# Kernel optimization log

Measured on AMD Instinct MI355X. Metric: run time of the kernel, lower is better.

Reference implementation:

```python
import jax, jax.numpy as jnp
import numpy as np

C, H, W = 64, 32, 32  # feature planes are (1, 64, 32, 32)
M = 1_048_576         # number of query points


def bilinear_sample(plane, coords):
    """torch.nn.functional.grid_sample, mode='bilinear', padding_mode='zeros',
    align_corners=True, for a single plane.
    plane: (C, H, W); coords: (M, 2) with (x, y) in [-1, 1] convention.
    Returns (M, C)."""
    c, h, w = plane.shape
    # align_corners=True mapping: -1 -> 0, +1 -> size-1
    x = (coords[:, 0] + 1.0) * 0.5 * (w - 1)
    y = (coords[:, 1] + 1.0) * 0.5 * (h - 1)
    x0 = jnp.floor(x)
    y0 = jnp.floor(y)
    wx1 = x - x0
    wy1 = y - y0
    wx0 = 1.0 - wx1
    wy0 = 1.0 - wy1

    def gather(xi, yi):
        xi = xi.astype(jnp.int32)
        yi = yi.astype(jnp.int32)
        valid = (xi >= 0) & (xi < w) & (yi >= 0) & (yi < h)  # zeros padding
        xc = jnp.clip(xi, 0, w - 1)
        yc = jnp.clip(yi, 0, h - 1)
        v = plane[:, yc, xc]  # (C, M)
        return jnp.where(valid[None, :], v, 0.0)

    out = (gather(x0, y0) * (wx0 * wy0)[None, :]
           + gather(x0 + 1, y0) * (wx1 * wy0)[None, :]
           + gather(x0, y0 + 1) * (wx0 * wy1)[None, :]
           + gather(x0 + 1, y0 + 1) * (wx1 * wy1)[None, :])
    return out.T  # (M, C)


def setup_inputs() -> dict:
    key = jax.random.key(0)
    ks = jax.random.split(key, 10)
    coordinates = jax.random.normal(ks[0], (1, M, 3), dtype=jnp.float32)
    # tri-plane embeddings: randn * 0.1, shape (1, C, H, W)
    plane_xy = jax.random.normal(ks[1], (1, C, H, W), dtype=jnp.float32) * 0.1
    plane_yz = jax.random.normal(ks[2], (1, C, H, W), dtype=jnp.float32) * 0.1
    plane_xz = jax.random.normal(ks[3], (1, C, H, W), dtype=jnp.float32) * 0.1
    # MLP 64 -> 128 -> 128 -> 1 (torch Linear weight shape = (out, in))
    # layer 0: first_layer_sine_init -> U(-1/64, 1/64)
    w1 = jax.random.uniform(ks[4], (128, 64), jnp.float32, -1.0 / 64, 1.0 / 64)
    b1 = jnp.zeros((128,), jnp.float32)
    # layers 1,2: frequency_init(30) -> U(-sqrt(6/in)/30, sqrt(6/in)/30)
    s2 = np.sqrt(6.0 / 128) / 30.0
    w2 = jax.random.uniform(ks[5], (128, 128), jnp.float32, -s2, s2)
    b2 = jnp.zeros((128,), jnp.float32)
    w3 = jax.random.uniform(ks[6], (1, 128), jnp.float32, -s2, s2)
    b3 = jnp.zeros((1,), jnp.float32)
    return {"coordinates": coordinates, "plane_xy": plane_xy, "plane_yz": plane_yz,
            "plane_xz": plane_xz, "w1": w1, "b1": b1, "w2": w2, "b2": b2,
            "w3": w3, "b3": b3}


def reference(coordinates, plane_xy, plane_yz, plane_xz, w1, b1, w2, b2, w3, b3):
    # coordinates: (1, M, 3); planes have leading batch dim of 1 (torch requires
    # grid batch == plane batch, so batch_size is structurally 1).
    samp = jax.vmap(bilinear_sample, in_axes=(None, 0))
    xy = samp(plane_xy[0], coordinates[..., 0:2])   # (1, M, C)
    yz = samp(plane_yz[0], coordinates[..., 1:3])   # (1, M, C)
    xz = samp(plane_xz[0], coordinates[..., ::2])   # (1, M, C)
    features = xy * yz * xz                          # aggregate_fn='prod'
    h = jax.nn.relu(jnp.einsum('bmc,oc->bmo', features, w1) + b1)
    h = jax.nn.relu(jnp.einsum('bmc,oc->bmo', h, w2) + b2)
    out = jnp.einsum('bmc,oc->bmo', h, w3) + b3      # (1, M, 1)
    return out
```

## Files before the change

### kernel.cpp

```cpp
#include <hip/hip_runtime.h>

#define MPTS 1048576

typedef _Float16 f16;
typedef _Float16 f16x4 __attribute__((ext_vector_type(4)));
typedef _Float16 f16x8 __attribute__((ext_vector_type(8)));
typedef float f32x4 __attribute__((ext_vector_type(4)));

static const size_t OFF_Z    = 0;
static const size_t OFF_CNT  = 64;
static const size_t OFF_PL   = 256;
static const size_t OFF_PLH  = OFF_PL + 786432;
static const size_t OFF_W1H  = OFF_PLH + 393216;
static const size_t OFF_W2H  = OFF_W1H + 16384;
static const size_t OFF_BCNT = OFF_W2H + 32768;
static const size_t OFF_BOFF = OFF_BCNT + 4096;
static const size_t OFF_LIST = OFF_BOFF + 4096;
static const size_t OFF_PC   = OFF_LIST + (size_t)MPTS*4;
static const size_t WS_LIST  = OFF_PC;
static const size_t WS_PC    = OFF_PC + (size_t)MPTS*16;

__device__ __forceinline__ int iclamp(int v, int lo, int hi) {
    return v < lo ? lo : (v > hi ? hi : v);
}
__device__ __forceinline__ int imin(int a, int b) { return a < b ? a : b; }

__device__ __forceinline__ bool isact(float x, float y, float z) {
    float px = fmaf(x, 15.5f, 15.5f);
    float py = fmaf(y, 15.5f, 15.5f);
    float pz = fmaf(z, 15.5f, 15.5f);
    return (px > -1.0f) & (px < 32.0f) & (py > -1.0f) & (py < 32.0f) &
           (pz > -1.0f) & (pz < 32.0f);
}

struct Bi { int o00, o01, o10, o11; float w00, w01, w10, w11; };

__device__ __forceinline__ Bi mkbi(float pa, float pb) {
    float fa = floorf(pa), fb = floorf(pb);
    int ia0 = (int)fa, ib0 = (int)fb;
    int ia1 = ia0 + 1, ib1 = ib0 + 1;
    float wa1 = pa - fa, wa0 = 1.0f - wa1;
    float wb1 = pb - fb, wb0 = 1.0f - wb1;
    float va0 = (ia0 >= 0 && ia0 < 32) ? wa0 : 0.0f;
    float va1 = (ia1 >= 0 && ia1 < 32) ? wa1 : 0.0f;
    float vb0 = (ib0 >= 0 && ib0 < 32) ? wb0 : 0.0f;
    float vb1 = (ib1 >= 0 && ib1 < 32) ? wb1 : 0.0f;
    int ca0 = iclamp(ia0, 0, 31), ca1 = iclamp(ia1, 0, 31);
    int cb0 = iclamp(ib0, 0, 31), cb1 = iclamp(ib1, 0, 31);
    Bi r;
    r.o00 = (cb0 * 32 + ca0) * 64; r.o01 = (cb0 * 32 + ca1) * 64;
    r.o10 = (cb1 * 32 + ca0) * 64; r.o11 = (cb1 * 32 + ca1) * 64;
    r.w00 = va0 * vb0; r.w01 = va1 * vb0; r.w10 = va0 * vb1; r.w11 = va1 * vb1;
    return r;
}

__device__ __forceinline__ float4 lerp4h(const f16* __restrict__ base,
                                         const int4 O, const float4 W) {
    f16x4 g00 = *(const f16x4*)(base + O.x);
    f16x4 g01 = *(const f16x4*)(base + O.y);
    f16x4 g10 = *(const f16x4*)(base + O.z);
    f16x4 g11 = *(const f16x4*)(base + O.w);
    float4 r;
    r.x = fmaf(W.x, (float)g00[0], fmaf(W.y, (float)g01[0], fmaf(W.z, (float)g10[0], W.w * (float)g11[0])));
    r.y = fmaf(W.x, (float)g00[1], fmaf(W.y, (float)g01[1], fmaf(W.z, (float)g10[1], W.w * (float)g11[1])));
    r.z = fmaf(W.x, (float)g00[2], fmaf(W.y, (float)g01[2], fmaf(W.z, (float)g10[2], W.w * (float)g11[2])));
    r.w = fmaf(W.x, (float)g00[3], fmaf(W.y, (float)g01[3], fmaf(W.z, (float)g10[3], W.w * (float)g11[3])));
    return r;
}

__device__ __forceinline__ void samp16(const float* __restrict__ pl,
                                       float pa, float pb, int c0,
                                       float* __restrict__ f, const bool mult) {
    Bi B = mkbi(pa, pb);
    const float4* p00 = (const float4*)(pl + B.o00 + c0);
    const float4* p01 = (const float4*)(pl + B.o01 + c0);
    const float4* p10 = (const float4*)(pl + B.o10 + c0);
    const float4* p11 = (const float4*)(pl + B.o11 + c0);
#pragma unroll
    for (int q = 0; q < 4; ++q) {
        float4 g00 = p00[q], g01 = p01[q], g10 = p10[q], g11 = p11[q];
        float vx = fmaf(B.w00, g00.x, fmaf(B.w01, g01.x, fmaf(B.w10, g10.x, B.w11 * g11.x)));
        float vy = fmaf(B.w00, g00.y, fmaf(B.w01, g01.y, fmaf(B.w10, g10.y, B.w11 * g11.y)));
        float vz = fmaf(B.w00, g00.z, fmaf(B.w01, g01.z, fmaf(B.w10, g10.z, B.w11 * g11.z)));
        float vw = fmaf(B.w00, g00.w, fmaf(B.w01, g01.w, fmaf(B.w10, g10.w, B.w11 * g11.w)));
        if (mult) {
            f[4*q+0] *= vx; f[4*q+1] *= vy; f[4*q+2] *= vz; f[4*q+3] *= vw;
        } else {
            f[4*q+0] = vx; f[4*q+1] = vy; f[4*q+2] = vz; f[4*q+3] = vw;
        }
    }
}

__global__ void k_prep(const float* __restrict__ pxy, const float* __restrict__ pyz,
                       const float* __restrict__ pxz,
                       const float* __restrict__ w1, const float* __restrict__ w2,
                       const float* __restrict__ b1, const float* __restrict__ b2,
                       const float* __restrict__ w3, const float* __restrict__ b3,
                       float* __restrict__ planes, f16* __restrict__ planes_h,
                       f16* __restrict__ w1h, f16* __restrict__ w2h,
                       float* __restrict__ zout) {
    if (blockIdx.x == 864) {
        int p = threadIdx.x;
        if (p >= 128) return;
        float h2p = b2[p];
        for (int o = 0; o < 128; ++o) h2p += w2[p * 128 + o] * fmaxf(b1[o], 0.0f);
        __shared__ float red[128];
        red[p] = fmaxf(h2p, 0.0f) * w3[p];
        __syncthreads();
        for (int s = 64; s > 0; s >>= 1) {
            if (p < s) red[p] += red[p + s];
            __syncthreads();
        }
        if (p == 0) *zout = red[0] + b3[0];
        return;
    }
    int tid = blockIdx.x * 256 + threadIdx.x;
    if (tid < 3 * 65536) {
        int t = tid >> 16;
        int r = tid & 65535;
        int hw = r >> 6;
        int c = r & 63;
        const float* src = (t == 0) ? pxy : ((t == 1) ? pyz : pxz);
        float v = src[c * 1024 + hw];
        planes[tid] = v;
        planes_h[tid] = (f16)v;
    } else if (tid < 3 * 65536 + 8192) {
        int r = tid - 3 * 65536;
        w1h[r] = (f16)w1[r];
    } else {
        int r = tid - (3 * 65536 + 8192);
        w2h[r] = (f16)w2[r];
    }
}

__global__ void k_count(const float* __restrict__ coords, const float* __restrict__ zptr,
                        int* __restrict__ bcnt, float* __restrict__ out) {
    int t = threadIdx.x, bid = blockIdx.x;
    const float4* c4 = (const float4*)coords + 768 * (size_t)bid + 3 * t;
    float4 a = c4[0], b = c4[1], c = c4[2];
    int base = bid * 1024 + t * 4;
    float z = *zptr;
    bool a0 = isact(a.x, a.y, a.z);
    bool a1 = isact(a.w, b.x, b.y);
    bool a2 = isact(b.z, b.w, c.x);
    bool a3 = isact(c.y, c.z, c.w);
    if (!a0) out[base + 0] = z;
    if (!a1) out[base + 1] = z;
    if (!a2) out[base + 2] = z;
    if (!a3) out[base + 3] = z;
    int s = (int)a0 + (int)a1 + (int)a2 + (int)a3;
#pragma unroll
    for (int off = 1; off <= 32; off <<= 1) s += __shfl_xor(s, off, 64);
    __shared__ int wt[4];
    if ((t & 63) == 0) wt[t >> 6] = s;
    __syncthreads();
    if (t == 0) bcnt[bid] = wt[0] + wt[1] + wt[2] + wt[3];
}

__global__ void k_scan(const int* __restrict__ bcnt, int* __restrict__ boff,
                       int* __restrict__ cnt) {
    int t = threadIdx.x, lane = t & 63, wv = t >> 6;
    int mine = bcnt[t];
    int incl = mine;
#pragma unroll
    for (int off = 1; off <= 32; off <<= 1) {
        int v = __shfl_up(incl, off, 64);
        if (lane >= off) incl += v;
    }
    __shared__ int wtot[16];
    if (lane == 63) wtot[wv] = incl;
    __syncthreads();
    int wexcl = 0;
#pragma unroll
    for (int k = 0; k < 16; ++k) wexcl += (k < wv) ? wtot[k] : 0;
    boff[t] = wexcl + incl - mine;
    if (t == 1023) *cnt = wexcl + incl;
}

template<bool PC>
__global__ void k_scatter(const float* __restrict__ coords, const int* __restrict__ boff,
                          int* __restrict__ list, float4* __restrict__ pc4) {
    int t = threadIdx.x, bid = blockIdx.x, lane = t & 63, wv = t >> 6;
    const float4* c4 = (const float4*)coords + 768 * (size_t)bid + 3 * t;
    float4 a = c4[0], b = c4[1], c = c4[2];
    int base = bid * 1024 + t * 4;
    float xs[4] = {a.x, a.w, b.z, c.y};
    float ys[4] = {a.y, b.x, b.w, c.z};
    float zs[4] = {a.z, b.y, c.x, c.w};
    bool act[4];
#pragma unroll
    for (int j = 0; j < 4; ++j) act[j] = isact(xs[j], ys[j], zs[j]);
    int mine = (int)act[0] + (int)act[1] + (int)act[2] + (int)act[3];
    int incl = mine;
#pragma unroll
    for (int off = 1; off <= 32; off <<= 1) {
        int v = __shfl_up(incl, off, 64);
        if (lane >= off) incl += v;
    }
    __shared__ int wtot[4];
    if (lane == 63) wtot[wv] = incl;
    __syncthreads();
    int wexcl = 0;
#pragma unroll
    for (int k = 0; k < 4; ++k) wexcl += (k < wv) ? wtot[k] : 0;
    int pos = boff[bid] + wexcl + incl - mine;
#pragma unroll
    for (int j = 0; j < 4; ++j) {
        if (act[j]) {
            list[pos] = base + j;
            if (PC) {
                float4 p;
                p.x = fmaf(xs[j], 15.5f, 15.5f);
                p.y = fmaf(ys[j], 15.5f, 15.5f);
                p.z = fmaf(zs[j], 15.5f, 15.5f);
                p.w = 0.0f;
                pc4[pos] = p;
            }
            ++pos;
        }
    }
}

__global__ __launch_bounds__(256, 2)
void k_fused(const float4* __restrict__ pc4, const f16* __restrict__ plh,
             const f16* __restrict__ w1h, const f16* __restrict__ w2h,
             const float* __restrict__ b1, const float* __restrict__ b2,
             const float* __restrict__ w3, const float* __restrict__ b3,
             const int* __restrict__ cnt, const int* __restrict__ list,
             float* __restrict__ out) {
    const int n = *cnt;
    const int tile = blockIdx.x;
    if (tile * 64 >= n) return;

    __shared__ __attribute__((aligned(16))) f16 Fs[64 * 64];
    __shared__ __attribute__((aligned(16))) f16 H1s[64 * 128];
    __shared__ float outp[4][64];
    __shared__ int4   BsO[64 * 3];
    __shared__ float4 BsW[64 * 3];

    const int t   = threadIdx.x;
    const int wv  = t >> 6;
    const int l   = t & 63;
    const int l15 = l & 15;
    const int lg  = l >> 4;
    const int ptw = t >> 4;
    const int cq  = t & 15;

    const float b3v = b3[0];

    if ((t & 3) < 3) {
        int pt0 = t >> 2;
        int pl  = t & 3;
        int ic = imin(tile * 64 + pt0, n - 1);
        float4 c = pc4[ic];
        float pa = (pl == 1) ? c.y : c.x;
        float pb = (pl == 0) ? c.y : c.z;
        Bi B = mkbi(pa, pb);
        BsO[pt0 * 3 + pl] = make_int4(B.o00, B.o01, B.o10, B.o11);
        BsW[pt0 * 3 + pl] = make_float4(B.w00, B.w01, B.w10, B.w11);
    }
    __syncthreads();

    const f16* bch = plh + cq * 4;
#pragma unroll
    for (int pass = 0; pass < 4; ++pass) {
        int pt = pass * 16 + ptw;
        float4 s0 = lerp4h(bch,          BsO[pt * 3 + 0], BsW[pt * 3 + 0]);
        float4 s1 = lerp4h(bch + 65536,  BsO[pt * 3 + 1], BsW[pt * 3 + 1]);
        float4 s2 = lerp4h(bch + 131072, BsO[pt * 3 + 2], BsW[pt * 3 + 2]);
        float4 f;
        f.x = (s0.x * s1.x) * s2.x;
        f.y = (s0.y * s1.y) * s2.y;
        f.z = (s0.z * s1.z) * s2.z;
        f.w = (s0.w * s1.w) * s2.w;
        f16x4 pk;
        pk[0] = (f16)f.x; pk[1] = (f16)f.y; pk[2] = (f16)f.z; pk[3] = (f16)f.w;
        *(f16x4*)((char*)Fs + pt * 128 + ((cq * 8) ^ ((pt & 7) << 4))) = pk;
    }
    __syncthreads();

    f16x8 af[4][2];
#pragma unroll
    for (int Mt = 0; Mt < 4; ++Mt) {
        int row = Mt * 16 + l15;
        const char* rb = (const char*)Fs + row * 128;
        int sw = (row & 7) << 4;
        af[Mt][0] = *(const f16x8*)(rb + ((lg * 16) ^ sw));
        af[Mt][1] = *(const f16x8*)(rb + ((64 + lg * 16) ^ sw));
    }

    f16x8 wf1[2][2];
    f16x8 wf2[2][4];
    f32x4 b1q[2], b2q[2], w3q[2];
#pragma unroll
    for (int ntl = 0; ntl < 2; ++ntl) {
        int nrow = (wv * 2 + ntl) * 16 + l15;
        wf1[ntl][0] = *(const f16x8*)(w1h + nrow * 64 + lg * 8);
        wf1[ntl][1] = *(const f16x8*)(w1h + nrow * 64 + 32 + lg * 8);
#pragma unroll
        for (int ks = 0; ks < 4; ++ks)
            wf2[ntl][ks] = *(const f16x8*)(w2h + nrow * 128 + ks * 32 + lg * 8);
        int nb = (wv * 2 + ntl) * 16 + lg * 4;
        b1q[ntl] = *(const f32x4*)(b1 + nb);
        b2q[ntl] = *(const f32x4*)(b2 + nb);
        w3q[ntl] = *(const f32x4*)(w3 + nb);
    }

    f32x4 acc[2][4];
#pragma unroll
    for (int ntl = 0; ntl < 2; ++ntl)
#pragma unroll
        for (int Mt = 0; Mt < 4; ++Mt) acc[ntl][Mt] = b1q[ntl];
    __builtin_amdgcn_s_setprio(1);
#pragma unroll
    for (int Mt = 0; Mt < 4; ++Mt) {
#pragma unroll
        for (int ntl = 0; ntl < 2; ++ntl) {
            acc[ntl][Mt] = __builtin_amdgcn_mfma_f32_16x16x32_f16(wf1[ntl][0], af[Mt][0], acc[ntl][Mt], 0, 0, 0);
            acc[ntl][Mt] = __builtin_amdgcn_mfma_f32_16x16x32_f16(wf1[ntl][1], af[Mt][1], acc[ntl][Mt], 0, 0, 0);
        }
    }
    __builtin_amdgcn_s_setprio(0);

#pragma unroll
    for (int ntl = 0; ntl < 2; ++ntl) {
#pragma unroll
        for (int Mt = 0; Mt < 4; ++Mt) {
            int pt = Mt * 16 + l15;
            int off = (((wv * 2 + ntl) * 32 + lg * 8) ^ ((pt & 7) << 4));
            f16x4 h;
            h[0] = (f16)fmaxf(acc[ntl][Mt][0], 0.0f);
            h[1] = (f16)fmaxf(acc[ntl][Mt][1], 0.0f);
            h[2] = (f16)fmaxf(acc[ntl][Mt][2], 0.0f);
            h[3] = (f16)fmaxf(acc[ntl][Mt][3], 0.0f);
            *(f16x4*)((char*)H1s + pt * 256 + off) = h;
        }
    }
    __syncthreads();

    f32x4 acc2[2][4];
#pragma unroll
    for (int ntl = 0; ntl < 2; ++ntl)
#pragma unroll
        for (int Mt = 0; Mt < 4; ++Mt) acc2[ntl][Mt] = b2q[ntl];
#pragma unroll
    for (int Mt = 0; Mt < 4; ++Mt) {
        int row = Mt * 16 + l15;
        const char* rb = (const char*)H1s + row * 256;
        int sw = (row & 7) << 4;
        f16x8 a0 = *(const f16x8*)(rb + ((lg * 16) ^ sw));
        f16x8 a1 = *(const f16x8*)(rb + ((64 + lg * 16) ^ sw));
        f16x8 a2 = *(const f16x8*)(rb + ((128 + lg * 16) ^ sw));
        f16x8 a3 = *(const f16x8*)(rb + ((192 + lg * 16) ^ sw));
        __builtin_amdgcn_s_setprio(1);
#pragma unroll
        for (int ntl = 0; ntl < 2; ++ntl) {
            acc2[ntl][Mt] = __builtin_amdgcn_mfma_f32_16x16x32_f16(wf2[ntl][0], a0, acc2[ntl][Mt], 0, 0, 0);
            acc2[ntl][Mt] = __builtin_amdgcn_mfma_f32_16x16x32_f16(wf2[ntl][1], a1, acc2[ntl][Mt], 0, 0, 0);
            acc2[ntl][Mt] = __builtin_amdgcn_mfma_f32_16x16x32_f16(wf2[ntl][2], a2, acc2[ntl][Mt], 0, 0, 0);
            acc2[ntl][Mt] = __builtin_amdgcn_mfma_f32_16x16x32_f16(wf2[ntl][3], a3, acc2[ntl][Mt], 0, 0, 0);
        }
        __builtin_amdgcn_s_setprio(0);
    }

#pragma unroll
    for (int Mt = 0; Mt < 4; ++Mt) {
        float s = 0.0f;
#pragma unroll
        for (int ntl = 0; ntl < 2; ++ntl)
#pragma unroll
            for (int r = 0; r < 4; ++r)
                s = fmaf(fmaxf(acc2[ntl][Mt][r], 0.0f), w3q[ntl][r], s);
        s += __shfl_xor(s, 16, 64);
        s += __shfl_xor(s, 32, 64);
        if (lg == 0) outp[wv][Mt * 16 + l15] = s;
    }
    __syncthreads();
    if (t < 64) {
        int gi = tile * 64 + t;
        if (gi < n) {
            float s = outp[0][t] + outp[1][t] + outp[2][t] + outp[3][t] + b3v;
            out[list[gi]] = s;
        }
    }
}

__global__ __launch_bounds__(256, 2)
void k_mlp(const float* __restrict__ coords, const float* __restrict__ planes,
           const f16* __restrict__ w1h, const f16* __restrict__ w2h,
           const float* __restrict__ b1, const float* __restrict__ b2,
           const float* __restrict__ w3, const float* __restrict__ b3,
           const int* __restrict__ cnt, const int* __restrict__ list,
           float* __restrict__ out) {
    const int n = *cnt;
    const int tile = blockIdx.x;
    if (tile * 64 >= n) return;

    __shared__ __attribute__((aligned(16))) f16 Fs[64 * 64];
    __shared__ __attribute__((aligned(16))) f16 H1s[64 * 128];
    __shared__ float outp[4][64];

    const int t   = threadIdx.x;
    const int wv  = t >> 6;
    const int l   = t & 63;
    const int l15 = l & 15;
    const int lg  = l >> 4;

    const float* pl0 = planes;
    const float* pl1 = planes + 65536;
    const float* pl2 = planes + 131072;

    f16x8 wf1[2][2];
    f16x8 wf2[2][4];
    float b1v[2], b2v[2], w3v[2];
#pragma unroll
    for (int ntl = 0; ntl < 2; ++ntl) {
        int nrow = (wv * 2 + ntl) * 16 + l15;
#pragma unroll
        for (int ks = 0; ks < 2; ++ks)
            wf1[ntl][ks] = *(const f16x8*)(w1h + nrow * 64 + ks * 32 + lg * 8);
#pragma unroll
        for (int ks = 0; ks < 4; ++ks)
            wf2[ntl][ks] = *(const f16x8*)(w2h + nrow * 128 + ks * 32 + lg * 8);
        b1v[ntl] = b1[nrow];
        b2v[ntl] = b2[nrow];
        w3v[ntl] = w3[nrow];
    }
    const float b3v = b3[0];

    {
        int pt = t >> 2, c0 = (t & 3) * 16;
        int ic = imin(tile * 64 + pt, n - 1);
        int i = list[ic];
        float px = fmaf(coords[3 * i + 0], 15.5f, 15.5f);
        float py = fmaf(coords[3 * i + 1], 15.5f, 15.5f);
        float pz = fmaf(coords[3 * i + 2], 15.5f, 15.5f);
        float feat[16];
        samp16(pl0, px, py, c0, feat, false);
        samp16(pl1, py, pz, c0, feat, true);
        samp16(pl2, px, pz, c0, feat, true);
        int sw = (pt & 7) << 4;
        char* Fb = (char*)Fs + pt * 128;
        f16x8 pk;
#pragma unroll
        for (int j = 0; j < 8; ++j) pk[j] = (f16)feat[j];
        *(f16x8*)(Fb + ((c0 * 2) ^ sw)) = pk;
#pragma unroll
        for (int j = 0; j < 8; ++j) pk[j] = (f16)feat[8 + j];
        *(f16x8*)(Fb + ((c0 * 2 + 16) ^ sw)) = pk;
    }
    __syncthreads();

    f32x4 acc[2][4];
#pragma unroll
    for (int ntl = 0; ntl < 2; ++ntl) {
        f32x4 ini = {b1v[ntl], b1v[ntl], b1v[ntl], b1v[ntl]};
#pragma unroll
        for (int Mt = 0; Mt < 4; ++Mt) acc[ntl][Mt] = ini;
    }
#pragma unroll
    for (int Mt = 0; Mt < 4; ++Mt) {
        int row = Mt * 16 + l15;
        const char* rb = (const char*)Fs + row * 128;
        int sw = (row & 7) << 4;
        f16x8 a0 = *(const f16x8*)(rb + ((lg * 16) ^ sw));
        f16x8 a1 = *(const f16x8*)(rb + ((64 + lg * 16) ^ sw));
#pragma unroll
        for (int ntl = 0; ntl < 2; ++ntl) {
            acc[ntl][Mt] = __builtin_amdgcn_mfma_f32_16x16x32_f16(a0, wf1[ntl][0], acc[ntl][Mt], 0, 0, 0);
            acc[ntl][Mt] = __builtin_amdgcn_mfma_f32_16x16x32_f16(a1, wf1[ntl][1], acc[ntl][Mt], 0, 0, 0);
        }
    }
#pragma unroll
    for (int ntl = 0; ntl < 2; ++ntl) {
        int ncol = (wv * 2 + ntl) * 16 + l15;
#pragma unroll
        for (int Mt = 0; Mt < 4; ++Mt) {
#pragma unroll
            for (int r = 0; r < 4; ++r) {
                int prow = Mt * 16 + lg * 4 + r;
                float v = fmaxf(acc[ntl][Mt][r], 0.0f);
                *(f16*)((char*)H1s + prow * 256 + ((ncol * 2) ^ ((prow & 7) << 4))) = (f16)v;
            }
        }
    }
    __syncthreads();

    f32x4 acc2[2][4];
#pragma unroll
    for (int ntl = 0; ntl < 2; ++ntl) {
        f32x4 ini = {b2v[ntl], b2v[ntl], b2v[ntl], b2v[ntl]};
#pragma unroll
        for (int Mt = 0; Mt < 4; ++Mt) acc2[ntl][Mt] = ini;
    }
#pragma unroll
    for (int Mt = 0; Mt < 4; ++Mt) {
        int row = Mt * 16 + l15;
        const char* rb = (const char*)H1s + row * 256;
        int sw = (row & 7) << 4;
        f16x8 a0 = *(const f16x8*)(rb + ((lg * 16) ^ sw));
        f16x8 a1 = *(const f16x8*)(rb + ((64 + lg * 16) ^ sw));
        f16x8 a2 = *(const f16x8*)(rb + ((128 + lg * 16) ^ sw));
        f16x8 a3 = *(const f16x8*)(rb + ((192 + lg * 16) ^ sw));
#pragma unroll
        for (int ntl = 0; ntl < 2; ++ntl) {
            acc2[ntl][Mt] = __builtin_amdgcn_mfma_f32_16x16x32_f16(a0, wf2[ntl][0], acc2[ntl][Mt], 0, 0, 0);
            acc2[ntl][Mt] = __builtin_amdgcn_mfma_f32_16x16x32_f16(a1, wf2[ntl][1], acc2[ntl][Mt], 0, 0, 0);
            acc2[ntl][Mt] = __builtin_amdgcn_mfma_f32_16x16x32_f16(a2, wf2[ntl][2], acc2[ntl][Mt], 0, 0, 0);
            acc2[ntl][Mt] = __builtin_amdgcn_mfma_f32_16x16x32_f16(a3, wf2[ntl][3], acc2[ntl][Mt], 0, 0, 0);
        }
    }

    float part[4][4];
#pragma unroll
    for (int Mt = 0; Mt < 4; ++Mt)
#pragma unroll
        for (int r = 0; r < 4; ++r)
            part[Mt][r] = fmaxf(acc2[0][Mt][r], 0.0f) * w3v[0] +
                          fmaxf(acc2[1][Mt][r], 0.0f) * w3v[1];
#pragma unroll
    for (int off = 1; off <= 8; off <<= 1) {
#pragma unroll
        for (int Mt = 0; Mt < 4; ++Mt)
#pragma unroll
            for (int r = 0; r < 4; ++r)
                part[Mt][r] += __shfl_xor(part[Mt][r], off, 64);
    }
    if (l15 == 0) {
#pragma unroll
        for (int Mt = 0; Mt < 4; ++Mt)
#pragma unroll
            for (int r = 0; r < 4; ++r)
                outp[wv][Mt * 16 + lg * 4 + r] = part[Mt][r];
    }
    __syncthreads();
    if (t < 64) {
        int gi = tile * 64 + t;
        if (gi < n) {
            float s = outp[0][t] + outp[1][t] + outp[2][t] + outp[3][t] + b3v;
            out[list[gi]] = s;
        }
    }
}

__global__ void k_fallback(const float* __restrict__ coords,
                           const float* __restrict__ p0, const float* __restrict__ p1,
                           const float* __restrict__ p2,
                           const float* __restrict__ w1, const float* __restrict__ b1,
                           const float* __restrict__ w2, const float* __restrict__ b2,
                           const float* __restrict__ w3, const float* __restrict__ b3,
                           float* __restrict__ out) {
    int i = blockIdx.x * 256 + threadIdx.x;
    if (i >= MPTS) return;
    float x = coords[3 * i + 0], y = coords[3 * i + 1], z = coords[3 * i + 2];
    float px = fmaf(x, 15.5f, 15.5f);
    float py = fmaf(y, 15.5f, 15.5f);
    float pz = fmaf(z, 15.5f, 15.5f);
    float feat[64];
    const float* pls[3] = {p0, p1, p2};
    float pa[3] = {px, py, px}, pb[3] = {py, pz, pz};
    for (int pidx = 0; pidx < 3; ++pidx) {
        float paf = pa[pidx], pbf = pb[pidx];
        float fa = floorf(paf), fb = floorf(pbf);
        int ia0 = (int)fa, ib0 = (int)fb, ia1 = ia0 + 1, ib1 = ib0 + 1;
        float wa1 = paf - fa, wa0 = 1.0f - wa1, wb1 = pbf - fb, wb0 = 1.0f - wb1;
        float va0 = (ia0 >= 0 && ia0 < 32) ? wa0 : 0.0f;
        float va1 = (ia1 >= 0 && ia1 < 32) ? wa1 : 0.0f;
        float vb0 = (ib0 >= 0 && ib0 < 32) ? wb0 : 0.0f;
        float vb1 = (ib1 >= 0 && ib1 < 32) ? wb1 : 0.0f;
        int ca0 = iclamp(ia0, 0, 31), ca1 = iclamp(ia1, 0, 31);
        int cb0 = iclamp(ib0, 0, 31), cb1 = iclamp(ib1, 0, 31);
        float w00 = va0 * vb0, w01 = va1 * vb0, w10 = va0 * vb1, w11 = va1 * vb1;
        int o00 = cb0 * 32 + ca0, o01 = cb0 * 32 + ca1;
        int o10 = cb1 * 32 + ca0, o11 = cb1 * 32 + ca1;
        const float* pl = pls[pidx];
        for (int c = 0; c < 64; ++c) {
            const float* pc = pl + c * 1024;
            float v = fmaf(w00, pc[o00], fmaf(w01, pc[o01],
                      fmaf(w10, pc[o10], w11 * pc[o11])));
            if (pidx == 0) feat[c] = v; else feat[c] *= v;
        }
    }
    float oa = b3[0];
    for (int half = 0; half < 2; ++half) {
        float h2h[64];
        for (int p = 0; p < 64; ++p) h2h[p] = b2[half * 64 + p];
        for (int o = 0; o < 128; ++o) {
            float a = b1[o];
            for (int c = 0; c < 64; ++c) a = fmaf(feat[c], w1[o * 64 + c], a);
            float r = fmaxf(a, 0.0f);
            for (int p = 0; p < 64; ++p) h2h[p] = fmaf(r, w2[(half * 64 + p) * 128 + o], h2h[p]);
        }
        for (int p = 0; p < 64; ++p) oa = fmaf(fmaxf(h2h[p], 0.0f), w3[half * 64 + p], oa);
    }
    out[i] = oa;
}

extern "C" void kernel_launch(void* const* d_in, const int* in_sizes, int n_in,
                              void* d_out, int out_size, void* d_ws, size_t ws_size,
                              hipStream_t stream) {
    const float* coords = (const float*)d_in[0];
    const float* pxy    = (const float*)d_in[1];
    const float* pyz    = (const float*)d_in[2];
    const float* pxz    = (const float*)d_in[3];
    const float* w1     = (const float*)d_in[4];
    const float* b1     = (const float*)d_in[5];
    const float* w2     = (const float*)d_in[6];
    const float* b2     = (const float*)d_in[7];
    const float* w3     = (const float*)d_in[8];
    const float* b3     = (const float*)d_in[9];
    float* out = (float*)d_out;

    if (ws_size >= WS_LIST) {
        float*  zout   = (float*)((char*)d_ws + OFF_Z);
        int*    cnt    = (int*)((char*)d_ws + OFF_CNT);
        float*  planes = (float*)((char*)d_ws + OFF_PL);
        f16*    plh    = (f16*)((char*)d_ws + OFF_PLH);
        f16*    w1h    = (f16*)((char*)d_ws + OFF_W1H);
        f16*    w2h    = (f16*)((char*)d_ws + OFF_W2H);
        int*    bcnt   = (int*)((char*)d_ws + OFF_BCNT);
        int*    boff   = (int*)((char*)d_ws + OFF_BOFF);
        int*    list   = (int*)((char*)d_ws + OFF_LIST);
        float4* pc4    = (float4*)((char*)d_ws + OFF_PC);

        k_prep<<<865, 256, 0, stream>>>(pxy, pyz, pxz, w1, w2, b1, b2, w3, b3,
                                        planes, plh, w1h, w2h, zout);
        k_count<<<1024, 256, 0, stream>>>(coords, zout, bcnt, out);
        k_scan<<<1, 1024, 0, stream>>>(bcnt, boff, cnt);

        if (ws_size >= WS_PC) {
            k_scatter<true><<<1024, 256, 0, stream>>>(coords, boff, list, pc4);
            k_fused<<<16384, 256, 0, stream>>>(pc4, plh, w1h, w2h,
                                               b1, b2, w3, b3, cnt, list, out);
        } else {
            k_scatter<false><<<1024, 256, 0, stream>>>(coords, boff, list, nullptr);
            k_mlp<<<16384, 256, 0, stream>>>(coords, planes, w1h, w2h,
                                             b1, b2, w3, b3, cnt, list, out);
        }
    } else {
        k_fallback<<<4096, 256, 0, stream>>>(coords, pxy, pyz, pxz,
                                             w1, b1, w2, b2, w3, b3, out);
    }
}
```

Before: 96.89 us.

## Store planes with x-neighbour interleaved and bilinear-sample via fdot2

The prep kernel now builds a duplicated fp16 plane layout where each texel stores its own value and its x+1 neighbour's value side by side per channel. The fused kernel then needs two 16-byte loads per plane per point instead of four 8-byte loads, and does the x-interpolation with packed fp16 dot products using weights packed as half2. This halves the gather count and cuts the conversion and FMA work, at the cost of doubling the plane footprint and holding the bilinear weights in fp16, which loses some accuracy.

```diff
diff --git a/kernel.cpp b/kernel.cpp
--- a/kernel.cpp
+++ b/kernel.cpp
@@ -3,6 +3,7 @@
 #define MPTS 1048576
 
 typedef _Float16 f16;
+typedef _Float16 f16x2 __attribute__((ext_vector_type(2)));
 typedef _Float16 f16x4 __attribute__((ext_vector_type(4)));
 typedef _Float16 f16x8 __attribute__((ext_vector_type(8)));
 typedef float f32x4 __attribute__((ext_vector_type(4)));
@@ -10,8 +11,8 @@
 static const size_t OFF_Z    = 0;
 static const size_t OFF_CNT  = 64;
 static const size_t OFF_PL   = 256;
-static const size_t OFF_PLH  = OFF_PL + 786432;
-static const size_t OFF_W1H  = OFF_PLH + 393216;
+static const size_t OFF_PLD  = OFF_PL + 786432;
+static const size_t OFF_W1H  = OFF_PLD + 786432;
 static const size_t OFF_W2H  = OFF_W1H + 16384;
 static const size_t OFF_BCNT = OFF_W2H + 32768;
 static const size_t OFF_BOFF = OFF_BCNT + 4096;
@@ -54,17 +55,18 @@
     return r;
 }
 
-__device__ __forceinline__ float4 lerp4h(const f16* __restrict__ base,
-                                         const int4 O, const float4 W) {
-    f16x4 g00 = *(const f16x4*)(base + O.x);
-    f16x4 g01 = *(const f16x4*)(base + O.y);
-    f16x4 g10 = *(const f16x4*)(base + O.z);
-    f16x4 g11 = *(const f16x4*)(base + O.w);
+__device__ __forceinline__ float4 lerp4d(const f16* __restrict__ base, const int4 P) {
+    f16x8 r0 = *(const f16x8*)(base + P.x);
+    f16x8 r1 = *(const f16x8*)(base + P.y);
+    f16x2 w0 = __builtin_bit_cast(f16x2, P.z);
+    f16x2 w1 = __builtin_bit_cast(f16x2, P.w);
+    const f16x2* a0 = (const f16x2*)&r0;
+    const f16x2* a1 = (const f16x2*)&r1;
     float4 r;
-    r.x = fmaf(W.x, (float)g00[0], fmaf(W.y, (float)g01[0], fmaf(W.z, (float)g10[0], W.w * (float)g11[0])));
-    r.y = fmaf(W.x, (float)g00[1], fmaf(W.y, (float)g01[1], fmaf(W.z, (float)g10[1], W.w * (float)g11[1])));
-    r.z = fmaf(W.x, (float)g00[2], fmaf(W.y, (float)g01[2], fmaf(W.z, (float)g10[2], W.w * (float)g11[2])));
-    r.w = fmaf(W.x, (float)g00[3], fmaf(W.y, (float)g01[3], fmaf(W.z, (float)g10[3], W.w * (float)g11[3])));
+    r.x = __builtin_amdgcn_fdot2(a0[0], w0, __builtin_amdgcn_fdot2(a1[0], w1, 0.0f, false), false);
+    r.y = __builtin_amdgcn_fdot2(a0[1], w0, __builtin_amdgcn_fdot2(a1[1], w1, 0.0f, false), false);
+    r.z = __builtin_amdgcn_fdot2(a0[2], w0, __builtin_amdgcn_fdot2(a1[2], w1, 0.0f, false), false);
+    r.w = __builtin_amdgcn_fdot2(a0[3], w0, __builtin_amdgcn_fdot2(a1[3], w1, 0.0f, false), false);
     return r;
 }
 
@@ -96,7 +98,7 @@
                        const float* __restrict__ w1, const float* __restrict__ w2,
                        const float* __restrict__ b1, const float* __restrict__ b2,
                        const float* __restrict__ w3, const float* __restrict__ b3,
-                       float* __restrict__ planes, f16* __restrict__ planes_h,
+                       float* __restrict__ planes, f16* __restrict__ dupl,
                        f16* __restrict__ w1h, f16* __restrict__ w2h,
                        float* __restrict__ zout) {
     if (blockIdx.x == 864) {
@@ -120,10 +122,15 @@
         int r = tid & 65535;
         int hw = r >> 6;
         int c = r & 63;
+        int y = hw >> 5, x = hw & 31;
+        int xp1 = imin(x + 1, 31);
         const float* src = (t == 0) ? pxy : ((t == 1) ? pyz : pxz);
-        float v = src[c * 1024 + hw];
+        float v  = src[c * 1024 + hw];
+        float v1 = src[c * 1024 + y * 32 + xp1];
         planes[tid] = v;
-        planes_h[tid] = (f16)v;
+        f16* d = dupl + (size_t)t * 131072 + hw * 128 + c * 2;
+        d[0] = (f16)v;
+        d[1] = (f16)v1;
     } else if (tid < 3 * 65536 + 8192) {
         int r = tid - 3 * 65536;
         w1h[r] = (f16)w1[r];
@@ -222,7 +229,7 @@
 }
 
 __global__ __launch_bounds__(256, 2)
-void k_fused(const float4* __restrict__ pc4, const f16* __restrict__ plh,
+void k_fused(const float4* __restrict__ pc4, const f16* __restrict__ dupl,
              const f16* __restrict__ w1h, const f16* __restrict__ w2h,
              const float* __restrict__ b1, const float* __restrict__ b2,
              const float* __restrict__ w3, const float* __restrict__ b3,
@@ -235,8 +242,7 @@
     __shared__ __attribute__((aligned(16))) f16 Fs[64 * 64];
     __shared__ __attribute__((aligned(16))) f16 H1s[64 * 128];
     __shared__ float outp[4][64];
-    __shared__ int4   BsO[64 * 3];
-    __shared__ float4 BsW[64 * 3];
+    __shared__ int4 BsP[64 * 3];
 
     const int t   = threadIdx.x;
     const int wv  = t >> 6;
@@ -255,19 +261,35 @@
         float4 c = pc4[ic];
         float pa = (pl == 1) ? c.y : c.x;
         float pb = (pl == 0) ? c.y : c.z;
-        Bi B = mkbi(pa, pb);
-        BsO[pt0 * 3 + pl] = make_int4(B.o00, B.o01, B.o10, B.o11);
-        BsW[pt0 * 3 + pl] = make_float4(B.w00, B.w01, B.w10, B.w11);
-    }
-    __syncthreads();
-
-    const f16* bch = plh + cq * 4;
+        float fa = floorf(pa), fb = floorf(pb);
+        int ia0 = (int)fa, ib0 = (int)fb;
+        float wa1 = pa - fa, wa0 = 1.0f - wa1;
+        float wb1 = pb - fb, wb0 = 1.0f - wb1;
+        float va0 = (ia0 >= 0 && ia0 < 32) ? wa0 : 0.0f;
+        float va1 = (ia0 + 1 >= 0 && ia0 + 1 < 32) ? wa1 : 0.0f;
+        float vb0 = (ib0 >= 0 && ib0 < 32) ? wb0 : 0.0f;
+        float vb1 = (ib0 + 1 >= 0 && ib0 + 1 < 32) ? wb1 : 0.0f;
+        int xb = iclamp(ia0, 0, 31);
+        float wx0 = (ia0 < 0) ? va1 : va0;
+        float wx1 = (ia0 < 0) ? 0.0f : va1;
+        int yb0 = iclamp(ib0, 0, 31), yb1 = iclamp(ib0 + 1, 0, 31);
+        f16x2 p0; p0[0] = (f16)(wx0 * vb0); p0[1] = (f16)(wx1 * vb0);
+        f16x2 p1; p1[0] = (f16)(wx0 * vb1); p1[1] = (f16)(wx1 * vb1);
+        int o0 = (yb0 * 32 + xb) * 128;
+        int o1 = (yb1 * 32 + xb) * 128;
+        BsP[pt0 * 3 + pl] = make_int4(o0, o1,
+                                      __builtin_bit_cast(int, p0),
+                                      __builtin_bit_cast(int, p1));
+    }
+    __syncthreads();
+
+    const f16* bch = dupl + cq * 8;
 #pragma unroll
     for (int pass = 0; pass < 4; ++pass) {
         int pt = pass * 16 + ptw;
-        float4 s0 = lerp4h(bch,          BsO[pt * 3 + 0], BsW[pt * 3 + 0]);
-        float4 s1 = lerp4h(bch + 65536,  BsO[pt * 3 + 1], BsW[pt * 3 + 1]);
-        float4 s2 = lerp4h(bch + 131072, BsO[pt * 3 + 2], BsW[pt * 3 + 2]);
+        float4 s0 = lerp4d(bch,          BsP[pt * 3 + 0]);
+        float4 s1 = lerp4d(bch + 131072, BsP[pt * 3 + 1]);
+        float4 s2 = lerp4d(bch + 262144, BsP[pt * 3 + 2]);
         float4 f;
         f.x = (s0.x * s1.x) * s2.x;
         f.y = (s0.y * s1.y) * s2.y;
@@ -615,7 +637,7 @@
         float*  zout   = (float*)((char*)d_ws + OFF_Z);
         int*    cnt    = (int*)((char*)d_ws + OFF_CNT);
         float*  planes = (float*)((char*)d_ws + OFF_PL);
-        f16*    plh    = (f16*)((char*)d_ws + OFF_PLH);
+        f16*    dupl   = (f16*)((char*)d_ws + OFF_PLD);
         f16*    w1h    = (f16*)((char*)d_ws + OFF_W1H);
         f16*    w2h    = (f16*)((char*)d_ws + OFF_W2H);
         int*    bcnt   = (int*)((char*)d_ws + OFF_BCNT);
@@ -624,13 +646,13 @@
         float4* pc4    = (float4*)((char*)d_ws + OFF_PC);
 
         k_prep<<<865, 256, 0, stream>>>(pxy, pyz, pxz, w1, w2, b1, b2, w3, b3,
-                                        planes, plh, w1h, w2h, zout);
+                                        planes, dupl, w1h, w2h, zout);
         k_count<<<1024, 256, 0, stream>>>(coords, zout, bcnt, out);
         k_scan<<<1, 1024, 0, stream>>>(bcnt, boff, cnt);
 
         if (ws_size >= WS_PC) {
             k_scatter<true><<<1024, 256, 0, stream>>>(coords, boff, list, pc4);
-            k_fused<<<16384, 256, 0, stream>>>(pc4, plh, w1h, w2h,
+            k_fused<<<16384, 256, 0, stream>>>(pc4, dupl, w1h, w2h,
                                                b1, b2, w3, b3, cnt, list, out);
         } else {
             k_scatter<false><<<1024, 256, 0, stream>>>(coords, boff, list, nullptr);
```

After: 83.97 us. 1.15x faster.
